# Kernel tuning notes

Measured on AMD Instinct MI355X. Metric: run time of the kernel, lower is better.

## Reference

```python
import jax, jax.numpy as jnp
import numpy as np

N = 100000   # nodes
E = 1600000  # edges
DIN = 128    # input features
H = 64       # hidden dim
C = 10       # classes
G = 512      # graphs in batch


def setup_inputs() -> dict:
    key = jax.random.key(0)
    ks = jax.random.split(key, 9)
    x = jax.random.normal(ks[0], (N, DIN), jnp.float32)
    edge_index = jax.random.randint(ks[1], (2, E), 0, N, dtype=jnp.int64)
    batch = jnp.sort(jax.random.randint(ks[2], (N,), 0, G, dtype=jnp.int64))
    W1 = jax.random.normal(ks[3], (DIN, H), jnp.float32) / np.sqrt(DIN).astype(np.float32)
    b1 = jnp.zeros((H,), jnp.float32)
    W2 = jax.random.normal(ks[4], (H, H), jnp.float32) / np.sqrt(H).astype(np.float32)
    b2 = jnp.zeros((H,), jnp.float32)
    Wl = jax.random.normal(ks[5], (H, C), jnp.float32) / np.sqrt(H).astype(np.float32)
    bl = jnp.zeros((C,), jnp.float32)
    return {"x": x, "edge_index": edge_index, "batch": batch,
            "W1": W1, "b1": b1, "W2": W2, "b2": b2, "Wl": Wl, "bl": bl}


def _gcn_conv(x, W, b, src, dst, norm):
    # transform then symmetric-normalized gather/scatter-add (PyG GCNConv)
    h = x @ W                          # [N, H]
    msg = h[src] * norm[:, None]       # [E+N, H] gather
    return jax.ops.segment_sum(msg, dst, num_segments=N) + b


def reference(x, edge_index, batch, W1, b1, W2, b2, Wl, bl):
    loop = jnp.arange(N, dtype=edge_index.dtype)
    src = jnp.concatenate([edge_index[0], loop])  # add self-loops
    dst = jnp.concatenate([edge_index[1], loop])
    deg = jax.ops.segment_sum(jnp.ones_like(dst, dtype=x.dtype), dst, num_segments=N)
    dinv = jnp.where(deg > 0, jax.lax.rsqrt(deg), 0.0)
    norm = dinv[src] * dinv[dst]                  # D^-1/2 (A+I) D^-1/2 weights

    h = jax.nn.relu(_gcn_conv(x, W1, b1, src, dst, norm))
    # dropout is identity in eval mode
    h = jax.nn.relu(_gcn_conv(h, W2, b2, src, dst, norm))

    counts = jax.ops.segment_sum(jnp.ones((N,), x.dtype), batch, num_segments=G)
    pooled = jax.ops.segment_sum(h, batch, num_segments=G) / jnp.maximum(counts, 1.0)[:, None]
    return pooled @ Wl + bl  # [G, C]
```

## Files before the change

kernel.cpp:

```cpp
#include <hip/hip_runtime.h>
#include <hip/hip_bf16.h>
#include <cstdint>

#define DIN 128
#define HD 64
#define NCLS 10
#define BSH 9
#define BIN_CHUNK 4096


__global__ __launch_bounds__(256)
void bucket_count_k(const int* __restrict__ dst, int* __restrict__ bktcnt,
                    int E, int nbkt) {
  __shared__ int h[256];
  const int t = threadIdx.x;
  h[t] = 0;
  __syncthreads();
  const int base = blockIdx.x * BIN_CHUNK;
  #pragma unroll
  for (int j = 0; j < 16; ++j) {
    int idx = base + j * 256 + t;
    if (idx < E) atomicAdd(&h[dst[idx] >> BSH], 1);
  }
  __syncthreads();
  if (t < nbkt && h[t]) atomicAdd(&bktcnt[t], h[t]);
}

__global__ __launch_bounds__(256)
void bucket_scan_k(const int* __restrict__ bktcnt, int* __restrict__ bktoff,
                   int* __restrict__ gcursor, int* __restrict__ rowstart,
                   int nbkt, int n, int E) {
  __shared__ int s[256];
  const int t = threadIdx.x;
  int v = (t < nbkt) ? bktcnt[t] : 0;
  s[t] = v;
  __syncthreads();
  for (int o = 1; o < 256; o <<= 1) {
    int u = (t >= o) ? s[t - o] : 0;
    __syncthreads();
    s[t] += u;
    __syncthreads();
  }
  int ex = s[t] - v;
  if (t < nbkt) { bktoff[t] = ex; gcursor[t] = ex; }
  if (t == 0)   { bktoff[nbkt] = E; rowstart[n] = E; }
}

__global__ __launch_bounds__(256)
void bin_k(const int* __restrict__ src, const int* __restrict__ dst,
           int* __restrict__ gcursor, unsigned int* __restrict__ binned,
           int E, int nbkt) {
  __shared__ int cnt[256], off[256], gb[256], s[256];
  __shared__ unsigned int pk_lds[BIN_CHUNK];
  __shared__ unsigned char sb[BIN_CHUNK];
  const int t = threadIdx.x;
  const int base = blockIdx.x * BIN_CHUNK;
  const int m = min(BIN_CHUNK, E - base);
  cnt[t] = 0;
  __syncthreads();
  unsigned int pk[16]; int bb[16]; int rk[16];
  #pragma unroll
  for (int j = 0; j < 16; ++j) {
    int idx = base + j * 256 + t;
    if (idx < E) {
      int d = dst[idx];
      int sv = src[idx];
      bb[j] = d >> BSH;
      pk[j] = ((unsigned)sv << BSH) | (unsigned)(d & ((1 << BSH) - 1));
      rk[j] = atomicAdd(&cnt[bb[j]], 1);
    } else bb[j] = -1;
  }
  __syncthreads();
  s[t] = cnt[t];
  __syncthreads();
  for (int o = 1; o < 256; o <<= 1) {
    int v = (t >= o) ? s[t - o] : 0;
    __syncthreads();
    s[t] += v;
    __syncthreads();
  }
  off[t] = s[t] - cnt[t];
  if (t < nbkt && cnt[t] > 0) gb[t] = atomicAdd(&gcursor[t], cnt[t]);
  __syncthreads();
  #pragma unroll
  for (int j = 0; j < 16; ++j) {
    if (bb[j] >= 0) {
      int p = off[bb[j]] + rk[j];
      pk_lds[p] = pk[j];
      sb[p] = (unsigned char)bb[j];
    }
  }
  __syncthreads();
  for (int i = t; i < m; i += 256) {
    int b = sb[i];
    binned[gb[b] + (i - off[b])] = pk_lds[i];
  }
}

__global__ __launch_bounds__(256)
void bucket_csr_k(const unsigned int* __restrict__ binned,
                  const int* __restrict__ bktoff,
                  int* __restrict__ rowstart, float* __restrict__ dinv,
                  int* __restrict__ csr_src, int n) {
  __shared__ int lcnt[512], loff[512], lcur[512], s[256];
  const int t = threadIdx.x;
  const int b = blockIdx.x;
  const int node0 = b << BSH;
  const int s0 = bktoff[b];
  const int e0 = bktoff[b + 1];
  const int cnt = e0 - s0;
  lcnt[t] = 0; lcnt[t + 256] = 0;
  lcur[t] = 0; lcur[t + 256] = 0;
  __syncthreads();
  for (int i = t; i < cnt; i += 256)
    atomicAdd(&lcnt[binned[s0 + i] & ((1 << BSH) - 1)], 1);
  __syncthreads();
  int a0 = lcnt[2 * t], a1 = lcnt[2 * t + 1];
  s[t] = a0 + a1;
  __syncthreads();
  for (int o = 1; o < 256; o <<= 1) {
    int v = (t >= o) ? s[t - o] : 0;
    __syncthreads();
    s[t] += v;
    __syncthreads();
  }
  int ex = s[t] - (a0 + a1);
  loff[2 * t] = ex;
  loff[2 * t + 1] = ex + a0;
  __syncthreads();
  #pragma unroll
  for (int i = t; i < 512; i += 256) {
    int node = node0 + i;
    if (node < n) {
      rowstart[node] = s0 + loff[i];
      dinv[node] = rsqrtf((float)(lcnt[i] + 1));
    }
  }
  for (int i = t; i < cnt; i += 256) {
    unsigned int pk = binned[s0 + i];
    int ld = pk & ((1 << BSH) - 1);
    int r = atomicAdd(&lcur[ld], 1);
    csr_src[s0 + loff[ld] + r] = (int)(pk >> BSH);
  }
}


template<int K>
__global__ __launch_bounds__(256)
void gemm_rowscale_k(const float* __restrict__ X, const float* __restrict__ W,
                     const float* __restrict__ dinv, __hip_bfloat16* __restrict__ out16,
                     int n) {
  __shared__ float sW[K * HD];
  __shared__ float sX[64 * 65];
  const int t  = threadIdx.x;
  const int tx = t & 15;
  const int ty = t >> 4;
  const int row0 = blockIdx.x * 64;

  for (int idx = t; idx < K * HD / 4; idx += 256)
    reinterpret_cast<float4*>(sW)[idx] = reinterpret_cast<const float4*>(W)[idx];

  float acc[4][4] = {};
  for (int kt = 0; kt < K; kt += 64) {
    __syncthreads();
    #pragma unroll
    for (int m = 0; m < 4; ++m) {
      int el = (m * 256 + t) * 4;
      int r = el >> 6, c = el & 63;
      float4 v;
      if (row0 + r < n) v = *reinterpret_cast<const float4*>(&X[(size_t)(row0 + r) * K + kt + c]);
      else              v = make_float4(0.f, 0.f, 0.f, 0.f);
      float* p = &sX[r * 65 + c];
      p[0] = v.x; p[1] = v.y; p[2] = v.z; p[3] = v.w;
    }
    __syncthreads();
    for (int k = 0; k < 64; ++k) {
      float4 w4 = *reinterpret_cast<const float4*>(&sW[(kt + k) * HD + tx * 4]);
      #pragma unroll
      for (int rr = 0; rr < 4; ++rr) {
        float a = sX[(ty * 4 + rr) * 65 + k];
        acc[rr][0] = fmaf(a, w4.x, acc[rr][0]);
        acc[rr][1] = fmaf(a, w4.y, acc[rr][1]);
        acc[rr][2] = fmaf(a, w4.z, acc[rr][2]);
        acc[rr][3] = fmaf(a, w4.w, acc[rr][3]);
      }
    }
  }
  #pragma unroll
  for (int rr = 0; rr < 4; ++rr) {
    int r = row0 + ty * 4 + rr;
    if (r < n) {
      float s = dinv[r];
      __hip_bfloat16 o[4];
      o[0] = __float2bfloat16(acc[rr][0] * s);
      o[1] = __float2bfloat16(acc[rr][1] * s);
      o[2] = __float2bfloat16(acc[rr][2] * s);
      o[3] = __float2bfloat16(acc[rr][3] * s);
      *reinterpret_cast<ushort4*>(&out16[(size_t)r * HD + tx * 4]) =
          *reinterpret_cast<ushort4*>(o);
    }
  }
}


__global__ __launch_bounds__(256)
void aggregate_k(const __hip_bfloat16* __restrict__ g, const int* __restrict__ rowstart,
                 const int* __restrict__ csr_src, const float* __restrict__ dinv,
                 const float* __restrict__ bias, float* __restrict__ out, int n) {
  const int lane = threadIdx.x & 63;
  const int hl   = lane & 31;
  const int wave = (blockIdx.x * 256 + threadIdx.x) >> 6;
  const int d    = wave * 2 + (lane >> 5);
  if (d >= n) return;
  const int p0 = rowstart[d], p1 = rowstart[d + 1];

  unsigned int v = *reinterpret_cast<const unsigned int*>(&g[(size_t)d * HD + hl * 2]);
  float ax = __uint_as_float(v << 16);
  float ay = __uint_as_float(v & 0xffff0000u);

  for (int p = p0; p < p1; p += 32) {
    const int nrem = p1 - p;
    int idx = (hl < nrem) ? csr_src[p + hl] : 0;
    #pragma unroll
    for (int j = 0; j < 32; ++j) {
      if (j < nrem) {
        int s = __shfl(idx, j, 32);
        unsigned int w = *reinterpret_cast<const unsigned int*>(&g[(size_t)s * HD + hl * 2]);
        ax += __uint_as_float(w << 16);
        ay += __uint_as_float(w & 0xffff0000u);
      }
    }
  }
  const float dv = dinv[d];
  float2 o;
  o.x = fmaxf(fmaf(dv, ax, bias[hl * 2]), 0.f);
  o.y = fmaxf(fmaf(dv, ay, bias[hl * 2 + 1]), 0.f);
  *reinterpret_cast<float2*>(&out[(size_t)d * HD + hl * 2]) = o;
}


__global__ __launch_bounds__(256)
void poolhead_k(const float* __restrict__ h, const int* __restrict__ batch,
                const float* __restrict__ Wl, const float* __restrict__ bl,
                float* __restrict__ outp, int n) {
  const int gi = blockIdx.x;
  const int lane = threadIdx.x & 63;
  const int w = threadIdx.x >> 6;
  int lo = 0, hi = n;
  while (lo < hi) { int mid = (lo + hi) >> 1; if (batch[mid] < gi) lo = mid + 1; else hi = mid; }
  const int start = lo;
  hi = n;
  while (lo < hi) { int mid = (lo + hi) >> 1; if (batch[mid] < gi + 1) lo = mid + 1; else hi = mid; }
  const int end = lo;
  float acc = 0.f;
  for (int i = start + w; i < end; i += 4) acc += h[(size_t)i * HD + lane];
  __shared__ float red[4][HD];
  __shared__ float pooled[HD];
  red[w][lane] = acc;
  __syncthreads();
  if (w == 0) {
    float s = red[0][lane] + red[1][lane] + red[2][lane] + red[3][lane];
    pooled[lane] = s / fmaxf((float)(end - start), 1.f);
  }
  __syncthreads();
  const int t = threadIdx.x;
  if (t < NCLS) {
    float s = bl[t];
    #pragma unroll
    for (int j = 0; j < HD; ++j) s = fmaf(pooled[j], Wl[j * NCLS + t], s);
    outp[gi * NCLS + t] = s;
  }
}


extern "C" void kernel_launch(void* const* d_in, const int* in_sizes, int n_in,
                              void* d_out, int out_size, void* d_ws, size_t ws_size,
                              hipStream_t stream) {
  const float* x   = (const float*)d_in[0];
  const int*   ei  = (const int*)d_in[1];
  const int* batch = (const int*)d_in[2];
  const float* W1  = (const float*)d_in[3];
  const float* b1  = (const float*)d_in[4];
  const float* W2  = (const float*)d_in[5];
  const float* b2  = (const float*)d_in[6];
  const float* Wl  = (const float*)d_in[7];
  const float* bl  = (const float*)d_in[8];
  const int N = in_sizes[0] / DIN;
  const int E = in_sizes[1] / 2;
  const int G = out_size / NCLS;
  const int* src = ei;
  const int* dst = ei + E;
  const int nbkt = (N + (1 << BSH) - 1) >> BSH;

  char* ws = (char*)d_ws;
  size_t off = 0;
  auto alloc = [&](size_t bytes) -> char* {
    char* p = ws + off;
    off += (bytes + 255) & ~size_t(255);
    return p;
  };
  int*   rowstart = (int*)alloc(sizeof(int) * (N + 1));
  int*   csr_src  = (int*)alloc(sizeof(int) * E);
  float* dinv     = (float*)alloc(sizeof(float) * N);
  __hip_bfloat16* A16 = (__hip_bfloat16*)alloc(sizeof(__hip_bfloat16) * (size_t)N * HD);
  float* B        = (float*)alloc(sizeof(float) * (size_t)N * HD);
  int*   bktcnt   = (int*)alloc(sizeof(int) * nbkt);
  int*   bktoff   = (int*)alloc(sizeof(int) * (nbkt + 1));
  int*   gcursor  = (int*)alloc(sizeof(int) * nbkt);
  unsigned int* binned = (unsigned int*)A16;

  const int nchunks = (E + BIN_CHUNK - 1) / BIN_CHUNK;
  hipMemsetAsync(bktcnt, 0, sizeof(int) * nbkt, stream);
  bucket_count_k<<<nchunks, 256, 0, stream>>>(dst, bktcnt, E, nbkt);
  bucket_scan_k<<<1, 256, 0, stream>>>(bktcnt, bktoff, gcursor, rowstart, nbkt, N, E);
  bin_k<<<nchunks, 256, 0, stream>>>(src, dst, gcursor, binned, E, nbkt);
  bucket_csr_k<<<nbkt, 256, 0, stream>>>(binned, bktoff, rowstart, dinv, csr_src, N);

  gemm_rowscale_k<DIN><<<(N + 63) / 64, 256, 0, stream>>>(x, W1, dinv, A16, N);
  aggregate_k<<<(N + 7) / 8, 256, 0, stream>>>(A16, rowstart, csr_src, dinv, b1, B, N);

  gemm_rowscale_k<HD><<<(N + 63) / 64, 256, 0, stream>>>(B, W2, dinv, A16, N);
  aggregate_k<<<(N + 7) / 8, 256, 0, stream>>>(A16, rowstart, csr_src, dinv, b2, B, N);

  poolhead_k<<<G, 256, 0, stream>>>(B, batch, Wl, bl, (float*)d_out, N);
}
```

Before: 349.2 us.

## Use bf16 MFMA for both GEMMs and store hidden activations in bf16

Replaces the scalar FP32 shared-memory GEMM with bf16 MFMA 16x16x32 kernels. Inputs and weights are converted to bf16 and staged in XOR-swizzled LDS. The aggregation output between layers is now written as bf16 rather than fp32, which halves that buffer's traffic for the second GEMM and the pooling pass. This costs some precision from bf16 rounding of the input features, the weights and the layer-1 activations.

Result: faster. 328.2 us (-6.0%).

```diff
diff --git a/kernel.cpp b/kernel.cpp
--- a/kernel.cpp
+++ b/kernel.cpp
@@ -7,6 +7,17 @@
 #define NCLS 10
 #define BSH 9
 #define BIN_CHUNK 4096
+
+typedef __bf16 bf16x8 __attribute__((ext_vector_type(8)));
+typedef float f32x4 __attribute__((ext_vector_type(4)));
+
+__device__ __forceinline__ unsigned short f2b(float f) {
+  unsigned int u = __float_as_uint(f);
+  return (unsigned short)((u + 0x7FFFu + ((u >> 16) & 1u)) >> 16);
+}
+__device__ __forceinline__ float b2f(unsigned short u) {
+  return __uint_as_float((unsigned int)u << 16);
+}
 
 
 __global__ __launch_bounds__(256)
@@ -145,68 +156,125 @@
 }
 
 
-template<int K>
-__global__ __launch_bounds__(256)
-void gemm_rowscale_k(const float* __restrict__ X, const float* __restrict__ W,
-                     const float* __restrict__ dinv, __hip_bfloat16* __restrict__ out16,
-                     int n) {
-  __shared__ float sW[K * HD];
-  __shared__ float sX[64 * 65];
-  const int t  = threadIdx.x;
-  const int tx = t & 15;
-  const int ty = t >> 4;
+__global__ __launch_bounds__(256)
+void gemm1_mfma_k(const float* __restrict__ X, const float* __restrict__ W,
+                  const float* __restrict__ dinv, unsigned short* __restrict__ out16,
+                  int n) {
+  __shared__ alignas(16) unsigned char sX[64 * 256];
+  __shared__ alignas(16) unsigned char sWT[64 * 256];
+  const int t = threadIdx.x;
+  const int lane = t & 63;
+  const int w = t >> 6;
   const int row0 = blockIdx.x * 64;
 
-  for (int idx = t; idx < K * HD / 4; idx += 256)
-    reinterpret_cast<float4*>(sW)[idx] = reinterpret_cast<const float4*>(W)[idx];
-
-  float acc[4][4] = {};
-  for (int kt = 0; kt < K; kt += 64) {
-    __syncthreads();
+  #pragma unroll
+  for (int i = 0; i < 8; ++i) {
+    int idx = i * 256 + t;
+    int r = idx >> 5, k = (idx & 31) * 4;
+    float4 v = make_float4(0.f, 0.f, 0.f, 0.f);
+    if (row0 + r < n) v = *reinterpret_cast<const float4*>(&X[(size_t)(row0 + r) * DIN + k]);
+    ushort4 bv = { f2b(v.x), f2b(v.y), f2b(v.z), f2b(v.w) };
+    *reinterpret_cast<ushort4*>(sX + ((r * 256 + k * 2) ^ ((r & 7) << 4))) = bv;
+  }
+  #pragma unroll
+  for (int i = 0; i < 32; ++i) {
+    int idx = i * 256 + t;
+    int k = idx >> 6, c = idx & 63;
+    *reinterpret_cast<unsigned short*>(sWT + ((c * 256 + k * 2) ^ ((c & 7) << 4))) =
+        f2b(W[k * HD + c]);
+  }
+  __syncthreads();
+
+  f32x4 acc[4];
+  #pragma unroll
+  for (int cb = 0; cb < 4; ++cb) acc[cb] = (f32x4){0.f, 0.f, 0.f, 0.f};
+  const int arow = w * 16 + (lane & 15);
+  const int kgrp = (lane >> 4) * 16;
+  #pragma unroll
+  for (int ks = 0; ks < 4; ++ks) {
+    bf16x8 a = *reinterpret_cast<bf16x8*>(sX + ((arow * 256 + ks * 64 + kgrp) ^ ((arow & 7) << 4)));
     #pragma unroll
-    for (int m = 0; m < 4; ++m) {
-      int el = (m * 256 + t) * 4;
-      int r = el >> 6, c = el & 63;
-      float4 v;
-      if (row0 + r < n) v = *reinterpret_cast<const float4*>(&X[(size_t)(row0 + r) * K + kt + c]);
-      else              v = make_float4(0.f, 0.f, 0.f, 0.f);
-      float* p = &sX[r * 65 + c];
-      p[0] = v.x; p[1] = v.y; p[2] = v.z; p[3] = v.w;
-    }
-    __syncthreads();
-    for (int k = 0; k < 64; ++k) {
-      float4 w4 = *reinterpret_cast<const float4*>(&sW[(kt + k) * HD + tx * 4]);
+    for (int cb = 0; cb < 4; ++cb) {
+      int col = cb * 16 + (lane & 15);
+      bf16x8 bfr = *reinterpret_cast<bf16x8*>(sWT + ((col * 256 + ks * 64 + kgrp) ^ ((col & 7) << 4)));
+      acc[cb] = __builtin_amdgcn_mfma_f32_16x16x32_bf16(a, bfr, acc[cb], 0, 0, 0);
+    }
+  }
+  const int rbase = row0 + w * 16 + (lane >> 4) * 4;
+  #pragma unroll
+  for (int j = 0; j < 4; ++j) {
+    int r = rbase + j;
+    if (r < n) {
+      float dv = dinv[r];
       #pragma unroll
-      for (int rr = 0; rr < 4; ++rr) {
-        float a = sX[(ty * 4 + rr) * 65 + k];
-        acc[rr][0] = fmaf(a, w4.x, acc[rr][0]);
-        acc[rr][1] = fmaf(a, w4.y, acc[rr][1]);
-        acc[rr][2] = fmaf(a, w4.z, acc[rr][2]);
-        acc[rr][3] = fmaf(a, w4.w, acc[rr][3]);
-      }
-    }
-  }
-  #pragma unroll
-  for (int rr = 0; rr < 4; ++rr) {
-    int r = row0 + ty * 4 + rr;
+      for (int cb = 0; cb < 4; ++cb)
+        out16[(size_t)r * HD + cb * 16 + (lane & 15)] = f2b(acc[cb][j] * dv);
+    }
+  }
+}
+
+
+__global__ __launch_bounds__(256)
+void gemm2_mfma_k(const unsigned short* __restrict__ B16, const float* __restrict__ W,
+                  const float* __restrict__ dinv, unsigned short* __restrict__ out16,
+                  int n) {
+  __shared__ alignas(16) unsigned char sX[64 * 128];
+  __shared__ alignas(16) unsigned char sWT[64 * 128];
+  const int t = threadIdx.x;
+  const int lane = t & 63;
+  const int w = t >> 6;
+  const int row0 = blockIdx.x * 64;
+
+  #pragma unroll
+  for (int i = 0; i < 4; ++i) {
+    int idx = i * 256 + t;
+    int r = idx >> 4, k = (idx & 15) * 4;
+    ushort4 v = make_ushort4(0, 0, 0, 0);
+    if (row0 + r < n) v = *reinterpret_cast<const ushort4*>(&B16[(size_t)(row0 + r) * HD + k]);
+    *reinterpret_cast<ushort4*>(sX + ((r * 128 + k * 2) ^ ((r & 7) << 4))) = v;
+  }
+  #pragma unroll
+  for (int i = 0; i < 16; ++i) {
+    int idx = i * 256 + t;
+    int k = idx >> 6, c = idx & 63;
+    *reinterpret_cast<unsigned short*>(sWT + ((c * 128 + k * 2) ^ ((c & 7) << 4))) =
+        f2b(W[k * HD + c]);
+  }
+  __syncthreads();
+
+  f32x4 acc[4];
+  #pragma unroll
+  for (int cb = 0; cb < 4; ++cb) acc[cb] = (f32x4){0.f, 0.f, 0.f, 0.f};
+  const int arow = w * 16 + (lane & 15);
+  const int kgrp = (lane >> 4) * 16;
+  #pragma unroll
+  for (int ks = 0; ks < 2; ++ks) {
+    bf16x8 a = *reinterpret_cast<bf16x8*>(sX + ((arow * 128 + ks * 64 + kgrp) ^ ((arow & 7) << 4)));
+    #pragma unroll
+    for (int cb = 0; cb < 4; ++cb) {
+      int col = cb * 16 + (lane & 15);
+      bf16x8 bfr = *reinterpret_cast<bf16x8*>(sWT + ((col * 128 + ks * 64 + kgrp) ^ ((col & 7) << 4)));
+      acc[cb] = __builtin_amdgcn_mfma_f32_16x16x32_bf16(a, bfr, acc[cb], 0, 0, 0);
+    }
+  }
+  const int rbase = row0 + w * 16 + (lane >> 4) * 4;
+  #pragma unroll
+  for (int j = 0; j < 4; ++j) {
+    int r = rbase + j;
     if (r < n) {
-      float s = dinv[r];
-      __hip_bfloat16 o[4];
-      o[0] = __float2bfloat16(acc[rr][0] * s);
-      o[1] = __float2bfloat16(acc[rr][1] * s);
-      o[2] = __float2bfloat16(acc[rr][2] * s);
-      o[3] = __float2bfloat16(acc[rr][3] * s);
-      *reinterpret_cast<ushort4*>(&out16[(size_t)r * HD + tx * 4]) =
-          *reinterpret_cast<ushort4*>(o);
-    }
-  }
-}
-
-
-__global__ __launch_bounds__(256)
-void aggregate_k(const __hip_bfloat16* __restrict__ g, const int* __restrict__ rowstart,
+      float dv = dinv[r];
+      #pragma unroll
+      for (int cb = 0; cb < 4; ++cb)
+        out16[(size_t)r * HD + cb * 16 + (lane & 15)] = f2b(acc[cb][j] * dv);
+    }
+  }
+}
+
+
+__global__ __launch_bounds__(256)
+void aggregate_k(const unsigned short* __restrict__ g, const int* __restrict__ rowstart,
                  const int* __restrict__ csr_src, const float* __restrict__ dinv,
-                 const float* __restrict__ bias, float* __restrict__ out, int n) {
+                 const float* __restrict__ bias, unsigned short* __restrict__ out16, int n) {
   const int lane = threadIdx.x & 63;
   const int hl   = lane & 31;
   const int wave = (blockIdx.x * 256 + threadIdx.x) >> 6;
@@ -225,22 +293,22 @@
     for (int j = 0; j < 32; ++j) {
       if (j < nrem) {
         int s = __shfl(idx, j, 32);
-        unsigned int w = *reinterpret_cast<const unsigned int*>(&g[(size_t)s * HD + hl * 2]);
-        ax += __uint_as_float(w << 16);
-        ay += __uint_as_float(w & 0xffff0000u);
+        unsigned int wv = *reinterpret_cast<const unsigned int*>(&g[(size_t)s * HD + hl * 2]);
+        ax += __uint_as_float(wv << 16);
+        ay += __uint_as_float(wv & 0xffff0000u);
       }
     }
   }
   const float dv = dinv[d];
-  float2 o;
-  o.x = fmaxf(fmaf(dv, ax, bias[hl * 2]), 0.f);
-  o.y = fmaxf(fmaf(dv, ay, bias[hl * 2 + 1]), 0.f);
-  *reinterpret_cast<float2*>(&out[(size_t)d * HD + hl * 2]) = o;
-}
-
-
-__global__ __launch_bounds__(256)
-void poolhead_k(const float* __restrict__ h, const int* __restrict__ batch,
+  float ox = fmaxf(fmaf(dv, ax, bias[hl * 2]), 0.f);
+  float oy = fmaxf(fmaf(dv, ay, bias[hl * 2 + 1]), 0.f);
+  unsigned int packed = ((unsigned int)f2b(oy) << 16) | (unsigned int)f2b(ox);
+  *reinterpret_cast<unsigned int*>(&out16[(size_t)d * HD + hl * 2]) = packed;
+}
+
+
+__global__ __launch_bounds__(256)
+void poolhead_k(const unsigned short* __restrict__ h16, const int* __restrict__ batch,
                 const float* __restrict__ Wl, const float* __restrict__ bl,
                 float* __restrict__ outp, int n) {
   const int gi = blockIdx.x;
@@ -253,7 +321,7 @@
   while (lo < hi) { int mid = (lo + hi) >> 1; if (batch[mid] < gi + 1) lo = mid + 1; else hi = mid; }
   const int end = lo;
   float acc = 0.f;
-  for (int i = start + w; i < end; i += 4) acc += h[(size_t)i * HD + lane];
+  for (int i = start + w; i < end; i += 4) acc += b2f(h16[(size_t)i * HD + lane]);
   __shared__ float red[4][HD];
   __shared__ float pooled[HD];
   red[w][lane] = acc;
@@ -302,8 +370,8 @@
   int*   rowstart = (int*)alloc(sizeof(int) * (N + 1));
   int*   csr_src  = (int*)alloc(sizeof(int) * E);
   float* dinv     = (float*)alloc(sizeof(float) * N);
-  __hip_bfloat16* A16 = (__hip_bfloat16*)alloc(sizeof(__hip_bfloat16) * (size_t)N * HD);
-  float* B        = (float*)alloc(sizeof(float) * (size_t)N * HD);
+  unsigned short* A16 = (unsigned short*)alloc(sizeof(unsigned short) * (size_t)N * HD);
+  unsigned short* B16 = (unsigned short*)alloc(sizeof(unsigned short) * (size_t)N * HD);
   int*   bktcnt   = (int*)alloc(sizeof(int) * nbkt);
   int*   bktoff   = (int*)alloc(sizeof(int) * (nbkt + 1));
   int*   gcursor  = (int*)alloc(sizeof(int) * nbkt);
@@ -316,11 +384,11 @@
   bin_k<<<nchunks, 256, 0, stream>>>(src, dst, gcursor, binned, E, nbkt);
   bucket_csr_k<<<nbkt, 256, 0, stream>>>(binned, bktoff, rowstart, dinv, csr_src, N);
 
-  gemm_rowscale_k<DIN><<<(N + 63) / 64, 256, 0, stream>>>(x, W1, dinv, A16, N);
-  aggregate_k<<<(N + 7) / 8, 256, 0, stream>>>(A16, rowstart, csr_src, dinv, b1, B, N);
-
-  gemm_rowscale_k<HD><<<(N + 63) / 64, 256, 0, stream>>>(B, W2, dinv, A16, N);
-  aggregate_k<<<(N + 7) / 8, 256, 0, stream>>>(A16, rowstart, csr_src, dinv, b2, B, N);
-
-  poolhead_k<<<G, 256, 0, stream>>>(B, batch, Wl, bl, (float*)d_out, N);
-}
+  gemm1_mfma_k<<<(N + 63) / 64, 256, 0, stream>>>(x, W1, dinv, A16, N);
+  aggregate_k<<<(N + 7) / 8, 256, 0, stream>>>(A16, rowstart, csr_src, dinv, b1, B16, N);
+
+  gemm2_mfma_k<<<(N + 63) / 64, 256, 0, stream>>>(B16, W2, dinv, A16, N);
+  aggregate_k<<<(N + 7) / 8, 256, 0, stream>>>(A16, rowstart, csr_src, dinv, b2, B16, N);
+
+  poolhead_k<<<G, 256, 0, stream>>>(B16, batch, Wl, bl, (float*)d_out, N);
+}
```
